# Kernel tuning notes

Measured on AMD Instinct MI355X. Metric: run time of the kernel, lower is better.

## Reference

```python
import jax, jax.numpy as jnp
import numpy as np

B, T, H, HW = 16, 32, 512, 32  # batch, timesteps, hidden channels, spatial size


def setup_inputs() -> dict:
    key = jax.random.key(0)
    k1, k2, k3, k4, k5 = jax.random.split(key, 5)
    x = jax.random.normal(k1, (B, T, HW, HW), dtype=jnp.float32)
    # cell conv: 1x1, (1 + H) -> 4H, with bias (k=1 default, padding 'same')
    W_conv = jax.random.normal(k2, (4 * H, 1 + H, 1, 1), dtype=jnp.float32) * 0.02
    b_conv = jax.random.normal(k3, (4 * H,), dtype=jnp.float32) * 0.02
    # post conv: 3x3, H -> 1, padding 'same'
    W_post = jax.random.normal(k4, (1, H, 3, 3), dtype=jnp.float32) * 0.02
    b_post = jax.random.normal(k5, (1,), dtype=jnp.float32) * 0.02
    return {"x": x, "W_conv": W_conv, "b_conv": b_conv, "W_post": W_post, "b_post": b_post}


def _post_conv(h, W_post, b_post):
    # NCHW 3x3 'same' conv
    y = jax.lax.conv_general_dilated(
        h, W_post, window_strides=(1, 1), padding="SAME",
        dimension_numbers=("NCHW", "OIHW", "NCHW"))
    return y + b_post[None, :, None, None]


def reference(x, W_conv, b_conv, W_post, b_post):
    Wc = W_conv[:, :, 0, 0]  # [4H, 1+H] -- 1x1 conv is a channel GEMM

    def step(carry, xt):
        h, c = carry  # [B,H,32,32] each; xt [B,1,32,32]
        z = jnp.concatenate([xt, h], axis=1)  # [B,1+H,32,32]
        gates = jnp.einsum("bchw,oc->bohw", z, Wc) + b_conv[None, :, None, None]
        i, f, o, g = jnp.split(gates, 4, axis=1)
        # Faithful to source (non-standard gating):
        c = jax.nn.sigmoid(f) * c + jax.nn.sigmoid(i) + jnp.tanh(g)
        h = jax.nn.sigmoid(o) + jnp.tanh(c)
        y = _post_conv(h, W_post, b_post)  # [B,1,32,32]
        return (h, c), y

    h0 = jnp.zeros((x.shape[0], H, HW, HW), dtype=x.dtype)
    c0 = jnp.zeros_like(h0)
    xs = x[:, :, None, :, :].transpose(1, 0, 2, 3, 4)  # [T,B,1,32,32]
    _, ys = jax.lax.scan(step, (h0, c0), xs)  # ys [T,B,1,32,32]
    out = ys[:, :, 0].transpose(1, 0, 2, 3)  # [B,T,32,32] == cat along dim=1
    return out
```

## Files before the change

kernel.cpp:

```cpp
#include <hip/hip_runtime.h>
#include <cstdint>
#include <cstddef>

#define B_    16
#define T_    32
#define H_    512
#define P_    1024
#define NPOS  16384
#define NG    2048

typedef __attribute__((ext_vector_type(8))) short short8;
typedef __attribute__((ext_vector_type(4))) float f32x4;

__device__ __forceinline__ unsigned short f2bf(float f) {
  uint32_t u = __float_as_uint(f);
  u += 0x7fffu + ((u >> 16) & 1u);
  return (unsigned short)(u >> 16);
}
__device__ __forceinline__ float bflo(uint32_t u) { return __uint_as_float(u << 16); }
__device__ __forceinline__ float bfhi(uint32_t u) { return __uint_as_float(u & 0xffff0000u); }

__device__ __forceinline__ float sigf(float x) {
  return __builtin_amdgcn_rcpf(1.0f + __expf(-x));
}
__device__ __forceinline__ float tanhf_(float x) {
  return 1.0f - 2.0f * __builtin_amdgcn_rcpf(__expf(2.0f * x) + 1.0f);
}

__device__ __forceinline__ void gload_lds16(const void* g, void* l) {
  __builtin_amdgcn_global_load_lds(
      (const __attribute__((address_space(1))) void*)g,
      (__attribute__((address_space(3))) void*)l, 16, 0, 0);
}

__global__ void repack_w(const float* __restrict__ Wc, const float* __restrict__ bconv,
                         unsigned short* __restrict__ Wp, float* __restrict__ w0x,
                         float* __restrict__ bx) {
  int idx = blockIdx.x * 256 + threadIdx.x;
  int r = idx >> 9, k = idx & 511;
  int ch = r >> 2, g = r & 3;
  int o = g * 512 + ch;
  Wp[idx] = f2bf(Wc[o * 513 + 1 + k]);
  if (k == 0) { w0x[r] = Wc[o * 513]; bx[r] = bconv[o]; }
}

__global__ void repack_wpost(const float* __restrict__ Wpost, unsigned short* __restrict__ wppb) {
  int idx = blockIdx.x * 256 + threadIdx.x;
  if (idx >= 16 * 512) return;
  int j = idx >> 9, c = idx & 511;
  float v = (j < 9) ? Wpost[c * 9 + j] : 0.f;
  unsigned short hi = f2bf(v);
  float lo = v - bflo((uint32_t)hi);
  wppb[idx] = hi;
  wppb[16 * 512 + idx] = f2bf(lo);
}

__global__ __launch_bounds__(256, 2)
void lstm_step(const unsigned short* __restrict__ Wp,
               const unsigned short* __restrict__ hprev,
               unsigned short* __restrict__ hnext,
               _Float16* __restrict__ Cst,
               const float* __restrict__ w0x, const float* __restrict__ bxv,
               const float* __restrict__ xin,
               const unsigned short* __restrict__ wppb,
               const float* __restrict__ uPrev, float* __restrict__ uCur,
               float* __restrict__ uNext,
               const float* __restrict__ bpost, float* __restrict__ out, int t) {
  __shared__ unsigned short As[256 * 64];
  __shared__ unsigned short Bs[128 * 64];

  const int tid = threadIdx.x;
  const int lane = tid & 63;
  const int wv = tid >> 6;
  const int wm = wv >> 1, wn = wv & 1;
  const int q = lane >> 4, l = lane & 15;

  const int lid = blockIdx.x;
  const int xcd = lid & 7;
  const int s   = lid >> 3;
  const int ny  = xcd * 16 + (s & 15);
  const int rx  = s >> 4;
  const int r0  = rx * 256;
  const int n0  = ny * 128;
  const int ch0 = rx * 64;

  const int srow = tid >> 3;
  const int lchunk = (tid & 7) ^ (srow & 7);
  const unsigned short* gA = Wp    + (size_t)(r0 + srow) * 512 + lchunk * 8;
  const unsigned short* gB = hprev + (size_t)(n0 + srow) * 512 + lchunk * 8;
  char* lA = (char*)As + wv * 1024;
  char* lB = (char*)Bs + wv * 1024;

  f32x4 acc[8][4] = {};

#pragma unroll
  for (int j = 0; j < 8; ++j)
    gload_lds16(gA + (size_t)j * (32 * 512), lA + j * 4096);
#pragma unroll
  for (int j = 0; j < 4; ++j)
    gload_lds16(gB + (size_t)j * (32 * 512), lB + j * 4096);

  if (t > 0 && tid < 16) {
    int pix = lid * 16 + tid;
    int b = pix >> 10, p = pix & 1023;
    int py = p >> 5, px = p & 31;
    float a = bpost[0];
#pragma unroll
    for (int dy = -1; dy <= 1; ++dy) {
      int nyy = py + dy;
      if ((unsigned)nyy > 31u) continue;
#pragma unroll
      for (int dx = -1; dx <= 1; ++dx) {
        int nx = px + dx;
        if ((unsigned)nx > 31u) continue;
        int j = (dy + 1) * 3 + (dx + 1);
        a += uPrev[j * NPOS + (b << 10) + (nyy << 5) + nx];
      }
    }
    out[((b * T_ + (t - 1)) << 10) + p] = a;
  }
  if (tid >= 16 && tid < 160)
    uNext[lid * 144 + (tid - 16)] = 0.f;

  for (int kc = 0; kc < 512; kc += 64) {
    __syncthreads();

#pragma unroll
    for (int kk = 0; kk < 2; ++kk) {
      short8 af[8], bf_[4];
#pragma unroll
      for (int mi = 0; mi < 8; ++mi) {
        int row = wm * 128 + mi * 16 + l;
        int sidx = row * 64 + (((kk * 4 + q) ^ (row & 7)) * 8);
        af[mi] = *(const short8*)(As + sidx);
      }
#pragma unroll
      for (int ni = 0; ni < 4; ++ni) {
        int row = wn * 64 + ni * 16 + l;
        int sidx = row * 64 + (((kk * 4 + q) ^ (row & 7)) * 8);
        bf_[ni] = *(const short8*)(Bs + sidx);
      }
#pragma unroll
      for (int mi = 0; mi < 8; ++mi)
#pragma unroll
        for (int ni = 0; ni < 4; ++ni)
          acc[mi][ni] = __builtin_amdgcn_mfma_f32_16x16x32_bf16(af[mi], bf_[ni], acc[mi][ni], 0, 0, 0);
    }
    __syncthreads();

    if (kc < 448) {
      int kn = kc + 64;
#pragma unroll
      for (int j = 0; j < 8; ++j)
        gload_lds16(gA + (size_t)j * (32 * 512) + kn, lA + j * 4096);
#pragma unroll
      for (int j = 0; j < 4; ++j)
        gload_lds16(gB + (size_t)j * (32 * 512) + kn, lB + j * 4096);
    }
  }

  float xv[4]; int posL[4]; size_t cbase[4];
#pragma unroll
  for (int ni = 0; ni < 4; ++ni) {
    posL[ni] = wn * 64 + ni * 16 + l;
    int pos = n0 + posL[ni];
    int b = pos >> 10, p = pos & 1023;
    xv[ni] = xin[((b * T_ + t) << 10) + p];
    cbase[ni] = ((size_t)b << 19) + p;
  }
#pragma unroll
  for (int mi = 0; mi < 8; ++mi) {
    int chl = wm * 32 + mi * 4 + q;
    int rg = r0 + wm * 128 + mi * 16 + q * 4;
    float4 w0 = *(const float4*)(w0x + rg);
    float4 bb = *(const float4*)(bxv + rg);
    int ch = ch0 + chl;
#pragma unroll
    for (int ni = 0; ni < 4; ++ni) {
      f32x4 g = acc[mi][ni];
      float gi = g[0] + w0.x * xv[ni] + bb.x;
      float gf = g[1] + w0.y * xv[ni] + bb.y;
      float go = g[2] + w0.z * xv[ni] + bb.z;
      float gg = g[3] + w0.w * xv[ni] + bb.w;
      size_t cidx = cbase[ni] + ((size_t)ch << 10);
      float cold = (float)Cst[cidx];
      float cn = sigf(gf) * cold + sigf(gi) + tanhf_(gg);
      float hn = sigf(go) + tanhf_(cn);
      Cst[cidx] = (_Float16)cn;
      As[posL[ni] * 64 + (chl ^ ((posL[ni] & 7) << 3))] = f2bf(hn);
    }
  }
  __syncthreads();

  {
    int pl = tid >> 1;
    int cb2 = (tid & 1) << 2;
    const unsigned short* srcrow = As + pl * 64;
    unsigned short* dst = hnext + (size_t)(n0 + pl) * 512 + ch0 + (cb2 << 3);
#pragma unroll
    for (int i = 0; i < 4; ++i)
      ((uint4*)dst)[i] = *(const uint4*)(srcrow + (((cb2 + i) ^ (pl & 7)) << 3));
  }

  {
    const unsigned short* wb_hi = wppb;
    const unsigned short* wb_lo = wppb + 16 * 512;
    const int posg = wv * 32;
    f32x4 a2[2] = {};
#pragma unroll
    for (int kk = 0; kk < 2; ++kk) {
      const int wo = l * 512 + ch0 + kk * 32 + q * 8;
      short8 whi = *(const short8*)(wb_hi + wo);
      short8 wlo = *(const short8*)(wb_lo + wo);
#pragma unroll
      for (int ni2 = 0; ni2 < 2; ++ni2) {
        int row = posg + ni2 * 16 + l;
        int sidx = row * 64 + (((kk * 4 + q) ^ (row & 7)) * 8);
        short8 hf = *(const short8*)(As + sidx);
        a2[ni2] = __builtin_amdgcn_mfma_f32_16x16x32_bf16(whi, hf, a2[ni2], 0, 0, 0);
        a2[ni2] = __builtin_amdgcn_mfma_f32_16x16x32_bf16(wlo, hf, a2[ni2], 0, 0, 0);
      }
    }
#pragma unroll
    for (int ni2 = 0; ni2 < 2; ++ni2) {
      int pix = n0 + posg + ni2 * 16 + l;
#pragma unroll
      for (int r = 0; r < 4; ++r) {
        int j = q * 4 + r;
        if (j < 9)
          unsafeAtomicAdd(&uCur[j * NPOS + pix], a2[ni2][r]);
      }
    }
  }
}

__global__ __launch_bounds__(256)
void conv_st(const float* __restrict__ u, const float* __restrict__ bpost,
             float* __restrict__ out, int t) {
  int idx = blockIdx.x * 256 + threadIdx.x;
  int b = idx >> 10, p = idx & 1023;
  int py = p >> 5, px = p & 31;
  float acc = bpost[0];
#pragma unroll
  for (int dy = -1; dy <= 1; ++dy) {
    int ny = py + dy;
    if ((unsigned)ny > 31u) continue;
#pragma unroll
    for (int dx = -1; dx <= 1; ++dx) {
      int nx = px + dx;
      if ((unsigned)nx > 31u) continue;
      int j = (dy + 1) * 3 + (dx + 1);
      acc += u[j * NPOS + (b << 10) + (ny << 5) + nx];
    }
  }
  out[((b * T_ + t) << 10) + p] = acc;
}

extern "C" void kernel_launch(void* const* d_in, const int* in_sizes, int n_in,
                              void* d_out, int out_size, void* d_ws, size_t ws_size,
                              hipStream_t stream) {
  const float* x     = (const float*)d_in[0];
  const float* Wconv = (const float*)d_in[1];
  const float* bconv = (const float*)d_in[2];
  const float* Wpost = (const float*)d_in[3];
  const float* bpost = (const float*)d_in[4];
  float* out = (float*)d_out;
  char* ws = (char*)d_ws;

  unsigned short* h0   = (unsigned short*)(ws);
  unsigned short* h1   = (unsigned short*)(ws + 16777216);
  _Float16*       Cst  = (_Float16*)(ws + 33554432);
  unsigned short* Wp   = (unsigned short*)(ws + 50331648);
  float*          w0x  = (float*)(ws + 52428800);
  float*          bx   = (float*)(ws + 52436992);
  unsigned short* wppb = (unsigned short*)(ws + 52445184);
  float*          u0   = (float*)(ws + 52477952);
  float*          u1   = (float*)(ws + 53067776);
  float*          u2   = (float*)(ws + 53657600);
  float* ub[3] = {u0, u1, u2};

  hipMemsetAsync(h0, 0, 16777216, stream);
  hipMemsetAsync(Cst, 0, 16777216, stream);
  hipMemsetAsync(u0, 0, 589824, stream);
  repack_w<<<4096, 256, 0, stream>>>(Wconv, bconv, Wp, w0x, bx);
  repack_wpost<<<32, 256, 0, stream>>>(Wpost, wppb);

  unsigned short* hp = h0;
  unsigned short* hn = h1;
  for (int t = 0; t < T_; ++t) {
    const float* uPrev = ub[(t + 2) % 3];
    float*       uCur  = ub[t % 3];
    float*       uNext = ub[(t + 1) % 3];
    lstm_step<<<1024, 256, 0, stream>>>(Wp, hp, hn, Cst, w0x, bx, x, wppb,
                                        uPrev, uCur, uNext, bpost, out, t);
    unsigned short* tmp = hp; hp = hn; hn = tmp;
  }
  conv_st<<<64, 256, 0, stream>>>(ub[(T_ - 1) % 3], bpost, out, T_ - 1);
}
```

Baseline: 1.746 ms.

## Double-buffer LDS K-loop with prefetch and fold log2e into gate weights

Splits the GEMM K loop into 32-wide steps with two LDS buffers, issuing the next tile's global-to-LDS loads before computing the current one so load latency overlaps MFMA work. It also drops one barrier per step. Gate weights and biases are pre-scaled by log2e (2·log2e for the tanh gate) so the activations use exp2 directly instead of a multiply plus exp. The change brings a new swizzle for the narrower tiles and slightly different bf16 rounding of the scaled weights.

After: 2.214 ms. 26.9% more time.

```diff
diff --git a/kernel.cpp b/kernel.cpp
--- a/kernel.cpp
+++ b/kernel.cpp
@@ -9,6 +9,9 @@
 #define NPOS  16384
 #define NG    2048
 
+#define LOG2E   1.442695041f
+#define LOG2E2  2.885390082f
+
 typedef __attribute__((ext_vector_type(8))) short short8;
 typedef __attribute__((ext_vector_type(4))) float f32x4;
 
@@ -20,11 +23,11 @@
 __device__ __forceinline__ float bflo(uint32_t u) { return __uint_as_float(u << 16); }
 __device__ __forceinline__ float bfhi(uint32_t u) { return __uint_as_float(u & 0xffff0000u); }
 
-__device__ __forceinline__ float sigf(float x) {
-  return __builtin_amdgcn_rcpf(1.0f + __expf(-x));
-}
-__device__ __forceinline__ float tanhf_(float x) {
-  return 1.0f - 2.0f * __builtin_amdgcn_rcpf(__expf(2.0f * x) + 1.0f);
+__device__ __forceinline__ float sig2(float y) {
+  return __builtin_amdgcn_rcpf(1.0f + exp2f(-y));
+}
+__device__ __forceinline__ float th2(float y) {
+  return 1.0f - 2.0f * __builtin_amdgcn_rcpf(exp2f(y) + 1.0f);
 }
 
 __device__ __forceinline__ void gload_lds16(const void* g, void* l) {
@@ -40,8 +43,9 @@
   int r = idx >> 9, k = idx & 511;
   int ch = r >> 2, g = r & 3;
   int o = g * 512 + ch;
-  Wp[idx] = f2bf(Wc[o * 513 + 1 + k]);
-  if (k == 0) { w0x[r] = Wc[o * 513]; bx[r] = bconv[o]; }
+  float s = (g == 3) ? LOG2E2 : LOG2E;
+  Wp[idx] = f2bf(Wc[o * 513 + 1 + k] * s);
+  if (k == 0) { w0x[r] = Wc[o * 513] * s; bx[r] = bconv[o] * s; }
 }
 
 __global__ void repack_wpost(const float* __restrict__ Wpost, unsigned short* __restrict__ wppb) {
@@ -66,8 +70,8 @@
                const float* __restrict__ uPrev, float* __restrict__ uCur,
                float* __restrict__ uNext,
                const float* __restrict__ bpost, float* __restrict__ out, int t) {
-  __shared__ unsigned short As[256 * 64];
-  __shared__ unsigned short Bs[128 * 64];
+  __shared__ unsigned short As2[2][256 * 32];
+  __shared__ unsigned short Bs2[2][128 * 32];
 
   const int tid = threadIdx.x;
   const int lane = tid & 63;
@@ -84,21 +88,26 @@
   const int n0  = ny * 128;
   const int ch0 = rx * 64;
 
-  const int srow = tid >> 3;
-  const int lchunk = (tid & 7) ^ (srow & 7);
-  const unsigned short* gA = Wp    + (size_t)(r0 + srow) * 512 + lchunk * 8;
-  const unsigned short* gB = hprev + (size_t)(n0 + srow) * 512 + lchunk * 8;
-  char* lA = (char*)As + wv * 1024;
-  char* lB = (char*)Bs + wv * 1024;
+  const int srow = tid >> 2;
+  const int gchunk = (tid & 3) ^ ((tid >> 3) & 3);
+  const unsigned short* gA = Wp    + (size_t)(r0 + srow) * 512 + gchunk * 8;
+  const unsigned short* gB = hprev + (size_t)(n0 + srow) * 512 + gchunk * 8;
+
+  auto stage = [&](int bb, int kt2) {
+    int kc = kt2 * 32;
+    char* lA = (char*)As2[bb] + wv * 1024;
+    char* lB = (char*)Bs2[bb] + wv * 1024;
+#pragma unroll
+    for (int j = 0; j < 4; ++j)
+      gload_lds16(gA + (size_t)(j * 64) * 512 + kc, lA + j * 4096);
+#pragma unroll
+    for (int j = 0; j < 2; ++j)
+      gload_lds16(gB + (size_t)(j * 64) * 512 + kc, lB + j * 4096);
+  };
 
   f32x4 acc[8][4] = {};
 
-#pragma unroll
-  for (int j = 0; j < 8; ++j)
-    gload_lds16(gA + (size_t)j * (32 * 512), lA + j * 4096);
-#pragma unroll
-  for (int j = 0; j < 4; ++j)
-    gload_lds16(gB + (size_t)j * (32 * 512), lB + j * 4096);
+  stage(0, 0);
 
   if (t > 0 && tid < 16) {
     int pix = lid * 16 + tid;
@@ -122,41 +131,34 @@
   if (tid >= 16 && tid < 160)
     uNext[lid * 144 + (tid - 16)] = 0.f;
 
-  for (int kc = 0; kc < 512; kc += 64) {
+  __syncthreads();
+
+  const int cxs = (q ^ ((l >> 1) & 3)) << 3;
+
+  for (int kt = 0; kt < 16; ++kt) {
+    const int cur = kt & 1;
+    if (kt < 15) stage(cur ^ 1, kt + 1);
+
+    const unsigned short* Ab = As2[cur];
+    const unsigned short* Bb = Bs2[cur];
+    short8 af[8], bf_[4];
+#pragma unroll
+    for (int mi = 0; mi < 8; ++mi) {
+      int row = wm * 128 + mi * 16 + l;
+      af[mi] = *(const short8*)(Ab + row * 32 + cxs);
+    }
+#pragma unroll
+    for (int ni = 0; ni < 4; ++ni) {
+      int row = wn * 64 + ni * 16 + l;
+      bf_[ni] = *(const short8*)(Bb + row * 32 + cxs);
+    }
+#pragma unroll
+    for (int mi = 0; mi < 8; ++mi)
+#pragma unroll
+      for (int ni = 0; ni < 4; ++ni)
+        acc[mi][ni] = __builtin_amdgcn_mfma_f32_16x16x32_bf16(af[mi], bf_[ni], acc[mi][ni], 0, 0, 0);
+
     __syncthreads();
-
-#pragma unroll
-    for (int kk = 0; kk < 2; ++kk) {
-      short8 af[8], bf_[4];
-#pragma unroll
-      for (int mi = 0; mi < 8; ++mi) {
-        int row = wm * 128 + mi * 16 + l;
-        int sidx = row * 64 + (((kk * 4 + q) ^ (row & 7)) * 8);
-        af[mi] = *(const short8*)(As + sidx);
-      }
-#pragma unroll
-      for (int ni = 0; ni < 4; ++ni) {
-        int row = wn * 64 + ni * 16 + l;
-        int sidx = row * 64 + (((kk * 4 + q) ^ (row & 7)) * 8);
-        bf_[ni] = *(const short8*)(Bs + sidx);
-      }
-#pragma unroll
-      for (int mi = 0; mi < 8; ++mi)
-#pragma unroll
-        for (int ni = 0; ni < 4; ++ni)
-          acc[mi][ni] = __builtin_amdgcn_mfma_f32_16x16x32_bf16(af[mi], bf_[ni], acc[mi][ni], 0, 0, 0);
-    }
-    __syncthreads();
-
-    if (kc < 448) {
-      int kn = kc + 64;
-#pragma unroll
-      for (int j = 0; j < 8; ++j)
-        gload_lds16(gA + (size_t)j * (32 * 512) + kn, lA + j * 4096);
-#pragma unroll
-      for (int j = 0; j < 4; ++j)
-        gload_lds16(gB + (size_t)j * (32 * 512) + kn, lB + j * 4096);
-    }
   }
 
   float xv[4]; int posL[4]; size_t cbase[4];
@@ -168,6 +170,7 @@
     xv[ni] = xin[((b * T_ + t) << 10) + p];
     cbase[ni] = ((size_t)b << 19) + p;
   }
+  unsigned short* stash = (unsigned short*)As2[0];
 #pragma unroll
   for (int mi = 0; mi < 8; ++mi) {
     int chl = wm * 32 + mi * 4 + q;
@@ -184,10 +187,10 @@
       float gg = g[3] + w0.w * xv[ni] + bb.w;
       size_t cidx = cbase[ni] + ((size_t)ch << 10);
       float cold = (float)Cst[cidx];
-      float cn = sigf(gf) * cold + sigf(gi) + tanhf_(gg);
-      float hn = sigf(go) + tanhf_(cn);
+      float cn = sig2(gf) * cold + sig2(gi) + th2(gg);
+      float hn = sig2(go) + th2(cn * LOG2E2);
       Cst[cidx] = (_Float16)cn;
-      As[posL[ni] * 64 + (chl ^ ((posL[ni] & 7) << 3))] = f2bf(hn);
+      stash[posL[ni] * 64 + (chl ^ ((posL[ni] & 7) << 3))] = f2bf(hn);
     }
   }
   __syncthreads();
@@ -195,7 +198,7 @@
   {
     int pl = tid >> 1;
     int cb2 = (tid & 1) << 2;
-    const unsigned short* srcrow = As + pl * 64;
+    const unsigned short* srcrow = stash + pl * 64;
     unsigned short* dst = hnext + (size_t)(n0 + pl) * 512 + ch0 + (cb2 << 3);
 #pragma unroll
     for (int i = 0; i < 4; ++i)
@@ -216,7 +219,7 @@
       for (int ni2 = 0; ni2 < 2; ++ni2) {
         int row = posg + ni2 * 16 + l;
         int sidx = row * 64 + (((kk * 4 + q) ^ (row & 7)) * 8);
-        short8 hf = *(const short8*)(As + sidx);
+        short8 hf = *(const short8*)(stash + sidx);
         a2[ni2] = __builtin_amdgcn_mfma_f32_16x16x32_bf16(whi, hf, a2[ni2], 0, 0, 0);
         a2[ni2] = __builtin_amdgcn_mfma_f32_16x16x32_bf16(wlo, hf, a2[ni2], 0, 0, 0);
       }
```
